# Kernel optimization log

Measured on AMD Instinct MI355X. Metric: run time of the kernel, lower is better.

The kernel has to match this reference:

```python
import jax, jax.numpy as jnp
import numpy as np

D, H = 256, 4            # model dim, num heads
HD = D // H              # head dim (even, needed by rotate_half)
B, N, M, NS = 2, 6, 512, 512  # batch, views, t keypoints, s keypoints
EPS = 1e-5


def _linear(x, w, b):
    return x @ w + b


def _ln(x, g, b):
    mu = x.mean(-1, keepdims=True)
    var = ((x - mu) ** 2).mean(-1, keepdims=True)
    return (x - mu) * jax.lax.rsqrt(var + EPS) * g + b


def _ffn(x, f1w, f1b, lng, lnb, f2w, f2b):
    # Linear(2d,2d) -> LayerNorm -> exact GELU -> Linear(2d,d)
    h = jax.nn.gelu(_ln(_linear(x, f1w, f1b), lng, lnb), approximate=False)
    return _linear(h, f2w, f2b)


def _rotate_half(x):
    # pairs (x0,x1) -> (-x1, x0), interleaved
    return jnp.stack((-x[..., 1::2], x[..., 0::2]), axis=-1).reshape(x.shape)


def _rope(freqs, t):
    return t * freqs[0] + _rotate_half(t) * freqs[1]


def _attn(q, k, v):
    sim = jnp.einsum('...id,...jd->...ij', q, k) * (q.shape[-1] ** -0.5)
    return jnp.einsum('...ij,...jd->...id', jax.nn.softmax(sim, axis=-1), v)


def _self_block(x, enc, qkv_w, qkv_b, out_w, out_b, *ffn_p):
    b, n_img, m, d = x.shape
    enc = jnp.swapaxes(enc, 2, 3)  # encoding.dim()==6 path
    qkv = _linear(x, qkv_w, qkv_b).reshape(b, n_img, m, H, HD, 3)
    qkv = jnp.swapaxes(qkv, -4, -3)  # [b,N,H,m,hd,3]
    q, k, v = qkv[..., 0], qkv[..., 1], qkv[..., 2]
    ctx = _attn(_rope(enc, q), _rope(enc, k), v)  # [b,N,H,m,hd]
    msg = _linear(jnp.swapaxes(ctx, -3, -2).reshape(b, n_img, m, d), out_w, out_b)
    return x + _ffn(jnp.concatenate([x, msg], -1), *ffn_p)


def _t2t_block(t, qkv_w, qkv_b, out_w, out_b, *ffn_p):
    t2 = jnp.swapaxes(t, 1, 2)  # [b,m,N,d]
    b, m, n_img, d = t2.shape
    qkv = _linear(t2, qkv_w, qkv_b).reshape(b, m, n_img, H, HD, 3)
    qkv = jnp.swapaxes(qkv, 3, 2)  # [b,m,H,N,hd,3]
    q, k, v = qkv[..., 0], qkv[..., 1], qkv[..., 2]
    ctx = _attn(q, k, v)  # [b,m,H,N,hd]
    msg = _linear(jnp.swapaxes(ctx, 3, 2).reshape(b, m, n_img, d), out_w, out_b)
    return jnp.swapaxes(t2 + _ffn(jnp.concatenate([t2, msg], -1), *ffn_p), 1, 2)


def _s2s_block(s, q_enc, k_enc, qkv_w, qkv_b, out_w, out_b, *ffn_p):
    b, n_img, n, d = s.shape
    qkv = _linear(s, qkv_w, qkv_b).reshape(b, n_img, n, H, HD, 3)
    qkv = jnp.swapaxes(jnp.swapaxes(qkv, -4, -3), -5, -4)  # [b,H,N,n,hd,3]
    q, k, v = qkv[..., 0], qkv[..., 1], qkv[..., 2]
    # expand queries across all views, RoPE per (i,j) view pair
    q = jnp.broadcast_to(q[:, :, None], (b, H, n_img, n_img, n, HD))
    q = _rope(q_enc, q).reshape(b, H, n_img, n_img * n, HD)
    k = _rope(k_enc, k)
    ctx = _attn(q, k, v).reshape(b, H, n_img, n_img, n, HD)
    # drop diagonal (i==j) entries exactly like boolean-mask indexing in torch
    off = np.nonzero(~np.eye(n_img, dtype=bool).ravel())[0]
    ctx = ctx.reshape(b, H, n_img * n_img, n, HD)[:, :, off]
    ctx = ctx.reshape(b, H, n_img - 1, n_img, n, HD).mean(2)  # [b,H,N,n,hd]
    ctx = jnp.swapaxes(jnp.swapaxes(ctx, 1, 2), 2, 3).reshape(b, n_img, n, d)
    msg = _linear(ctx, out_w, out_b)
    return s + _ffn(jnp.concatenate([s, msg], -1), *ffn_p)


def _cross_block(d0, d1, q_w, q_b, kv_w, kv_b, out_w, out_b, *ffn_p):
    b, n_img, m, d = d0.shape
    m1 = d1.shape[2]
    q = jnp.swapaxes(_linear(d0, q_w, q_b).reshape(b, n_img, m, H, HD), 2, 3)
    kv = jnp.swapaxes(_linear(d1, kv_w, kv_b).reshape(b, n_img, m1, H, HD, 2), 2, 3)
    ctx = _attn(q, kv[..., 0], kv[..., 1])  # [b,N,H,m,hd]
    msg = _linear(jnp.swapaxes(ctx, 2, 3).reshape(b, n_img, m, d), out_w, out_b)
    return d0 + _ffn(jnp.concatenate([d0, msg], -1), *ffn_p)


def setup_inputs() -> dict:
    key = jax.random.key(0)
    ks = iter(jax.random.split(key, 80))
    f32 = jnp.float32

    def lin(din, dout):
        return (jax.random.normal(next(ks), (din, dout), f32) * (din ** -0.5),
                jnp.zeros((dout,), f32))

    inp = {}
    inp['t_desc'] = jax.random.normal(next(ks), (B, N, M, D), f32)
    inp['s_desc'] = jax.random.normal(next(ks), (B, N, NS, D), f32)
    inp['t_encoding'] = jax.random.normal(next(ks), (2, 1, 1, N, M, HD), f32)
    inp['s_encoding'] = jax.random.normal(next(ks), (2, 1, 1, N, NS, HD), f32)
    inp['q_encoding'] = jax.random.normal(next(ks), (2, 1, 1, N, N, 1, HD), f32)
    inp['k_encoding'] = jax.random.normal(next(ks), (2, 1, 1, N, NS, HD), f32)
    for pre in ('sa', 'ss', 'tt'):
        inp[pre + '_qkv_w'], inp[pre + '_qkv_b'] = lin(D, 3 * D)
        inp[pre + '_out_w'], inp[pre + '_out_b'] = lin(D, D)
        inp[pre + '_f1_w'], inp[pre + '_f1_b'] = lin(2 * D, 2 * D)
        inp[pre + '_ln_g'] = jnp.ones((2 * D,), f32)
        inp[pre + '_ln_b'] = jnp.zeros((2 * D,), f32)
        inp[pre + '_f2_w'], inp[pre + '_f2_b'] = lin(2 * D, D)
    inp['ca_q_w'], inp['ca_q_b'] = lin(D, D)
    inp['ca_kv_w'], inp['ca_kv_b'] = lin(D, 2 * D)
    inp['ca_out_w'], inp['ca_out_b'] = lin(D, D)
    inp['ca_f1_w'], inp['ca_f1_b'] = lin(2 * D, 2 * D)
    inp['ca_ln_g'] = jnp.ones((2 * D,), f32)
    inp['ca_ln_b'] = jnp.zeros((2 * D,), f32)
    inp['ca_f2_w'], inp['ca_f2_b'] = lin(2 * D, D)
    inp['cf_w1'], inp['cf_b1'] = lin(D, D)
    inp['cf_w2'], inp['cf_b2'] = lin(D, 1)
    return inp


def reference(t_desc, s_desc, t_encoding, s_encoding, q_encoding, k_encoding,
              sa_qkv_w, sa_qkv_b, sa_out_w, sa_out_b, sa_f1_w, sa_f1_b, sa_ln_g, sa_ln_b, sa_f2_w, sa_f2_b,
              ss_qkv_w, ss_qkv_b, ss_out_w, ss_out_b, ss_f1_w, ss_f1_b, ss_ln_g, ss_ln_b, ss_f2_w, ss_f2_b,
              tt_qkv_w, tt_qkv_b, tt_out_w, tt_out_b, tt_f1_w, tt_f1_b, tt_ln_g, tt_ln_b, tt_f2_w, tt_f2_b,
              ca_q_w, ca_q_b, ca_kv_w, ca_kv_b, ca_out_w, ca_out_b, ca_f1_w, ca_f1_b, ca_ln_g, ca_ln_b, ca_f2_w, ca_f2_b,
              cf_w1, cf_b1, cf_w2, cf_b2):
    sa = (sa_qkv_w, sa_qkv_b, sa_out_w, sa_out_b, sa_f1_w, sa_f1_b, sa_ln_g, sa_ln_b, sa_f2_w, sa_f2_b)
    t = _self_block(t_desc, t_encoding, *sa)   # shared SelfBlock weights
    s = _self_block(s_desc, s_encoding, *sa)
    t = _t2t_block(t, tt_qkv_w, tt_qkv_b, tt_out_w, tt_out_b, tt_f1_w, tt_f1_b, tt_ln_g, tt_ln_b, tt_f2_w, tt_f2_b)
    s = _s2s_block(s, q_encoding, k_encoding, ss_qkv_w, ss_qkv_b, ss_out_w, ss_out_b, ss_f1_w, ss_f1_b, ss_ln_g, ss_ln_b, ss_f2_w, ss_f2_b)
    ca = (ca_q_w, ca_q_b, ca_kv_w, ca_kv_b, ca_out_w, ca_out_b, ca_f1_w, ca_f1_b, ca_ln_g, ca_ln_b, ca_f2_w, ca_f2_b)
    t2 = _cross_block(t, s, *ca)               # shared CrossBlock weights
    s2 = _cross_block(s, t, *ca)
    conf = _linear(jax.nn.relu(_linear(jax.lax.stop_gradient(s), cf_w1, cf_b1)), cf_w2, cf_b2)[..., 0]
    return t2, s2, conf
```

## Files before the change

kernel.cpp:

```cpp
#include <hip/hip_runtime.h>
#include <hip/hip_bf16.h>
#include <math.h>

constexpr int kD   = 256;
constexpr int kH   = 4;
constexpr int kHD  = 64;
constexpr int kB   = 2;
constexpr int kN   = 6;
constexpr int kM   = 512;
constexpr int kRowsH = kB*kN*kM;
constexpr int kRows  = 2*kRowsH;
constexpr int kGrpH  = kB*kN*kH;
constexpr int kGrp   = 2*kGrpH;
constexpr size_t kTOK = (size_t)kRowsH*kD;
constexpr size_t kEncSlab = (size_t)kN*kM*kHD;
constexpr size_t kQEncSlab = (size_t)kN*kN*kHD;
constexpr float kL2E = 1.4426950408889634f;

typedef unsigned short u16;
typedef __attribute__((ext_vector_type(8))) short s16x8;
typedef __attribute__((ext_vector_type(4))) float f32x4;

__device__ __forceinline__ float wred_sum(float v){
  #pragma unroll
  for (int m=32;m>0;m>>=1) v += __shfl_xor(v, m, 64);
  return v;
}
__device__ __forceinline__ u16 f2b(float x){
  union { float f; unsigned u; } a; a.f = x;
  unsigned r = a.u + 0x7fffu + ((a.u >> 16) & 1u);
  return (u16)(r >> 16);
}
__device__ __forceinline__ float b2f(u16 x){
  union { unsigned u; float f; } a; a.u = ((unsigned)x) << 16;
  return a.f;
}
__device__ __forceinline__ unsigned pk2(float lo, float hi){
  union { __hip_bfloat162 h2; unsigned u; } c;
  c.h2 = __float22bfloat162_rn(make_float2(lo, hi));
  return c.u;
}

struct FuseArgs {
  const float* Wout[4]; const float* W1[4];
  const float* bout[4]; const float* b1[4];
  float* Wtmp; float* b1p;
};

__global__ __launch_bounds__(256) void wfuse_k(FuseArgs fa)
{
  if (blockIdx.x >= 128) {
    const int bb = blockIdx.x - 128;
    const int set = bb >> 1;
    const int n = (bb & 1)*256 + threadIdx.x;
    const float* W1 = fa.W1[set];
    const float* bo = fa.bout[set];
    float s = fa.b1[set][n];
    for (int k = 0; k < 256; ++k)
      s = fmaf(bo[k], W1[(size_t)(256+k)*512 + n], s);
    fa.b1p[set*512 + n] = s;
    return;
  }
  const int set = blockIdx.x >> 5;
  const int t = blockIdx.x & 31;
  const int row0 = (t >> 3)*64, col0 = (t & 7)*64;
  const float* A  = fa.Wout[set];
  const float* Bm = fa.W1[set] + 256*512;
  float* C = fa.Wtmp + (size_t)set*(256*512);
  __shared__ float As[16][65];
  __shared__ float Bs[16][64];
  const int tid = threadIdx.x;
  const int tx = tid & 15, ty = tid >> 4;
  const int ar = tid >> 2, ak = (tid & 3)*4;
  const int wr = tid >> 4, wc = (tid & 15)*4;
  float acc[4][4] = {};
  for (int kt = 0; kt < 256; kt += 16) {
    float4 av = *(const float4*)(A + (size_t)(row0+ar)*256 + kt + ak);
    As[ak+0][ar]=av.x; As[ak+1][ar]=av.y; As[ak+2][ar]=av.z; As[ak+3][ar]=av.w;
    *(float4*)(&Bs[wr][wc]) = *(const float4*)(Bm + (size_t)(kt+wr)*512 + col0 + wc);
    __syncthreads();
    #pragma unroll
    for (int k2=0;k2<16;++k2) {
      float a[4], b[4];
      #pragma unroll
      for (int i=0;i<4;++i) a[i]=As[k2][ty*4+i];
      #pragma unroll
      for (int j=0;j<4;++j) b[j]=Bs[k2][tx*4+j];
      #pragma unroll
      for (int i=0;i<4;++i)
        #pragma unroll
        for (int j=0;j<4;++j) acc[i][j] = fmaf(a[i], b[j], acc[i][j]);
    }
    __syncthreads();
  }
  #pragma unroll
  for (int i=0;i<4;++i)
    #pragma unroll
    for (int j=0;j<4;++j)
      C[(size_t)(row0+ty*4+i)*512 + col0+tx*4+j] = acc[i][j];
}

struct WtDesc { const float* W; const float* W2; u16* Wt; int K; int N; int ntiles; };
struct WtTable { WtDesc d[18]; };

__global__ __launch_bounds__(256) void wtcast_k(WtTable tab)
{
  int t = blockIdx.x, mi = 0;
  while (t >= tab.d[mi].ntiles) { t -= tab.d[mi].ntiles; ++mi; }
  const float* W = tab.d[mi].W;
  const float* W2 = tab.d[mi].W2;
  u16* Wt = tab.d[mi].Wt;
  const int K = tab.d[mi].K, N = tab.d[mi].N;
  const int ktn = K >> 5;
  const int nt = t / ktn, kt = t % ktn;
  const int n0 = nt*128, k0 = kt*32;
  u16* dst = Wt + (size_t)t*4096;
  #pragma unroll
  for (int s = 0; s < 2; ++s) {
    const int idx0 = (s*256 + (int)threadIdx.x)*8;
    const int ar = idx0 >> 5;
    const int w8 = (idx0 >> 3) & 3;
    const int sw = (ar >> 1) & 3;
    int kk = k0 + ((w8 ^ sw) << 3);
    const int n  = n0 + ar;
    const float* src = W;
    if (W2 && kk >= 256) { src = W2; kk -= 256; }
    union { u16 u[8]; s16x8 v; } o;
    #pragma unroll
    for (int e = 0; e < 8; ++e)
      o.u[e] = f2b(src[(size_t)(kk + e)*N + n]);
    *(s16x8*)(dst + idx0) = o.v;
  }
}

template<bool A1B, bool A2B, bool CB>
__global__ __launch_bounds__(256) void mmad_k(
    const void* __restrict__ A1a, const void* __restrict__ A1b,
    const void* __restrict__ A2a, const void* __restrict__ A2b, int K1,
    const u16* __restrict__ Wa, const u16* __restrict__ Wb,
    const float* __restrict__ bia, const float* __restrict__ bib,
    const float* __restrict__ bi2a, const float* __restrict__ bi2b, int Ns,
    const float* __restrict__ Ra, const float* __restrict__ Rb,
    void* __restrict__ Cp, int N, int K, int Mh, int doRelu)
{
  __shared__ u16 As[2][128*32];
  __shared__ u16 Bs[2][128*32];
  const int tid = threadIdx.x;
  const int lane = tid & 63, w = tid >> 6;
  const int gx = gridDim.x;
  const int nblk = gx * gridDim.y;
  int flat = blockIdx.y*gx + blockIdx.x;
  if (!(nblk & 7)) flat = (flat & 7)*(nblk >> 3) + (flat >> 3);
  const int bxx = flat % gx, byy = flat / gx;
  const int row0 = byy*128, col0 = bxx*128;
  const bool sec = (row0 >= Mh);
  const int lr0 = sec ? row0 - Mh : row0;
  const void* A1 = sec ? A1b : A1a;
  const void* A2 = sec ? A2b : A2a;
  const u16* Wt  = sec ? Wb : Wa;
  const float* bias  = sec ? bib : bia;
  const float* bias2 = sec ? bi2b : bi2a;
  const float* R = sec ? Rb : Ra;
  const int wr = (w >> 1)*64, wc = (w & 1)*64;
  const int ar = tid >> 1, ah = tid & 1;
  const int K2 = K - K1;
  const int ktn = K >> 5;
  f32x4 acc[4][4] = {};

  auto stage = [&](int buf, int kt) {
    const u16* wtile = Wt + ((size_t)((col0 >> 7)*ktn + (kt >> 5)))*4096;
    #pragma unroll
    for (int s = 0; s < 2; ++s) {
      const u16* srcp = wtile + (size_t)(s*256 + tid)*8;
      __builtin_amdgcn_global_load_lds(
          (const __attribute__((address_space(1))) void*)srcp,
          (__attribute__((address_space(3))) void*)((char*)Bs[buf] + s*4096 + w*1024),
          16, 0, 0);
    }
    const int kk = kt + ah*16;
    union { u16 u[16]; s16x8 v[2]; } tmp;
    if (kk < K1) {
      if constexpr (A1B) {
        const u16* ap = (const u16*)A1 + (size_t)(lr0+ar)*K1 + kk;
        tmp.v[0] = *(const s16x8*)ap; tmp.v[1] = *(const s16x8*)(ap+8);
      } else {
        const float* ap = (const float*)A1 + (size_t)(lr0+ar)*K1 + kk;
        #pragma unroll
        for (int i = 0; i < 16; i += 4) {
          f32x4 v4 = *(const f32x4*)(ap + i);
          tmp.u[i+0]=f2b(v4.x); tmp.u[i+1]=f2b(v4.y); tmp.u[i+2]=f2b(v4.z); tmp.u[i+3]=f2b(v4.w);
        }
      }
    } else {
      if constexpr (A2B) {
        const u16* ap = (const u16*)A2 + (size_t)(lr0+ar)*K2 + (kk - K1);
        tmp.v[0] = *(const s16x8*)ap; tmp.v[1] = *(const s16x8*)(ap+8);
      } else {
        const float* ap = (const float*)A2 + (size_t)(lr0+ar)*K2 + (kk - K1);
        #pragma unroll
        for (int i = 0; i < 16; i += 4) {
          f32x4 v4 = *(const f32x4*)(ap + i);
          tmp.u[i+0]=f2b(v4.x); tmp.u[i+1]=f2b(v4.y); tmp.u[i+2]=f2b(v4.z); tmp.u[i+3]=f2b(v4.w);
        }
      }
    }
    const int sw = (ar >> 1) & 3;
    *(s16x8*)(&As[buf][ar*32 + ((ah*2+0)^sw)*8]) = tmp.v[0];
    *(s16x8*)(&As[buf][ar*32 + ((ah*2+1)^sw)*8]) = tmp.v[1];
  };

  stage(0, 0);
  __syncthreads();
  for (int t = 0; t < ktn; ++t) {
    const int cur = t & 1;
    if (t + 1 < ktn) stage(cur ^ 1, (t + 1) << 5);
    s16x8 af[4], bfv[4];
    #pragma unroll
    for (int fm = 0; fm < 4; ++fm) {
      const int r = wr + fm*16 + (lane & 15);
      const int g = (lane >> 4) ^ ((r >> 1) & 3);
      af[fm] = *(const s16x8*)(&As[cur][r*32 + g*8]);
    }
    #pragma unroll
    for (int fn = 0; fn < 4; ++fn) {
      const int c = wc + fn*16 + (lane & 15);
      const int g = (lane >> 4) ^ ((c >> 1) & 3);
      bfv[fn] = *(const s16x8*)(&Bs[cur][c*32 + g*8]);
    }
    #pragma unroll
    for (int fm = 0; fm < 4; ++fm)
      #pragma unroll
      for (int fn = 0; fn < 4; ++fn)
        acc[fm][fn] = __builtin_amdgcn_mfma_f32_16x16x32_bf16(af[fm], bfv[fn], acc[fm][fn], 0, 0, 0);
    __syncthreads();
  }

  #pragma unroll
  for (int fm = 0; fm < 4; ++fm) {
    const int ro = wr + fm*16 + (lane >> 4)*4;
    #pragma unroll
    for (int fn = 0; fn < 4; ++fn) {
      const int cc = col0 + wc + fn*16 + (lane & 15);
      const float bv = (cc < Ns) ? bias[cc] : bias2[cc - Ns];
      #pragma unroll
      for (int j = 0; j < 4; ++j) {
        float v = acc[fm][fn][j] + bv;
        if (R) v += R[(size_t)(lr0 + ro + j)*N + cc];
        if (doRelu) v = fmaxf(v, 0.f);
        const size_t idx = (size_t)(row0 + ro + j)*N + cc;
        if constexpr (CB) ((u16*)Cp)[idx] = f2b(v);
        else              ((float*)Cp)[idx] = v;
      }
    }
  }
}

__global__ __launch_bounds__(256) void prep_self_k(
    const u16* __restrict__ qkvU, const float* __restrict__ t_enc,
    const float* __restrict__ s_enc,
    u16* __restrict__ Qb, u16* __restrict__ Kb, u16* __restrict__ Vt)
{
  __shared__ u16 vs[64][66];
  const int g = blockIdx.x >> 3, i0 = (blockIdx.x & 7)*64;
  const int h = g & 3, bn = g >> 2;
  const float* enc = (bn < 12) ? t_enc : s_enc;
  const int n = (bn < 12 ? bn : bn - 12) % kN;
  const int c = threadIdx.x & 63, t4 = threadIdx.x >> 6;
  const float sgn = (c & 1) ? 1.f : -1.f;
  #pragma unroll 4
  for (int rr = 0; rr < 16; ++rr) {
    const int il = rr*4 + t4, i = i0 + il;
    const u16* base = qkvU + ((size_t)bn*kM + i)*768 + h*192;
    const float q = b2f(base[c*3]), k = b2f(base[c*3+1]);
    const float qp = b2f(base[(c^1)*3]), kp = b2f(base[(c^1)*3+1]);
    const size_t eo = ((size_t)(n*kM + i))*kHD + c;
    const float e0 = enc[eo], e1 = enc[kEncSlab + eo];
    Qb[((size_t)g*kM + i)*kHD + c] = f2b((q*e0 + sgn*qp*e1)*0.125f);
    Kb[((size_t)g*kM + i)*kHD + c] = f2b(k*e0 + sgn*kp*e1);
    vs[il][c] = base[c*3+2];
  }
  __syncthreads();
  #pragma unroll 4
  for (int rr = 0; rr < 16; ++rr) {
    const int cc = rr*4 + t4;
    Vt[((size_t)g*kHD + cc)*kM + i0 + c] = vs[c][cc];
  }
}

__global__ __launch_bounds__(256) void prep_s2s_k(
    const u16* __restrict__ qkvU, const float* __restrict__ kenc,
    float* __restrict__ Qs, u16* __restrict__ Kb, u16* __restrict__ Vt)
{
  __shared__ u16 vs[64][66];
  const int g = blockIdx.x >> 3, i0 = (blockIdx.x & 7)*64;
  const int view = g % kN, bh = g / kN;
  const int h = bh & 3, b = bh >> 2;
  const int c = threadIdx.x & 63, t4 = threadIdx.x >> 6;
  const float sgn = (c & 1) ? 1.f : -1.f;
  #pragma unroll 4
  for (int rr = 0; rr < 16; ++rr) {
    const int il = rr*4 + t4, i = i0 + il;
    const u16* base = qkvU + ((size_t)(kRowsH + (b*kN+view)*kM + i))*768 + h*192;
    const float k = b2f(base[c*3+1]), kp = b2f(base[(c^1)*3+1]);
    const size_t eo = ((size_t)(view*kM + i))*kHD + c;
    const float e0 = kenc[eo], e1 = kenc[kEncSlab + eo];
    Qs[((size_t)g*kM + i)*kHD + c] = b2f(base[c*3]);
    Kb[((size_t)g*kM + i)*kHD + c] = f2b(k*e0 + sgn*kp*e1);
    vs[il][c] = base[c*3+2];
  }
  __syncthreads();
  #pragma unroll 4
  for (int rr = 0; rr < 16; ++rr) {
    const int cc = rr*4 + t4;
    Vt[((size_t)g*kHD + cc)*kM + i0 + c] = vs[c][cc];
  }
}

__global__ __launch_bounds__(256) void prep_cross_k(
    const u16* __restrict__ qkvC, u16* __restrict__ Kb, u16* __restrict__ Vt)
{
  __shared__ u16 vs[64][66];
  const int g = blockIdx.x >> 3, i0 = (blockIdx.x & 7)*64;
  const int h = g & 3, bn = g >> 2;
  const int src = (bn < 12) ? bn + 12 : bn - 12;
  const int c = threadIdx.x & 63, t4 = threadIdx.x >> 6;
  #pragma unroll 4
  for (int rr = 0; rr < 16; ++rr) {
    const int il = rr*4 + t4, i = i0 + il;
    const u16* base = qkvC + ((size_t)src*kM + i)*768 + 256 + h*128;
    Kb[((size_t)g*kM + i)*kHD + c] = f2b(b2f(base[c*2]) * 0.125f);
    vs[il][c] = base[c*2+1];
  }
  __syncthreads();
  #pragma unroll 4
  for (int rr = 0; rr < 16; ++rr) {
    const int cc = rr*4 + t4;
    Vt[((size_t)g*kHD + cc)*kM + i0 + c] = vs[c][cc];
  }
}

template<int CROSSQ>
__global__ __launch_bounds__(256) void attn_mm_k(
    const u16* __restrict__ Qb, const u16* __restrict__ Kb,
    const u16* __restrict__ Vt, u16* __restrict__ ctx)
{
  const int w = threadIdx.x >> 6, lane = threadIdx.x & 63;
  const int bij = (blockIdx.x & 7)*48 + (blockIdx.x >> 3);
  const int g = bij >> 2, qblk = bij & 3;
  const int h = g & 3, bn = g >> 2;
  const int q0 = qblk*128 + w*32;
  const int qr = lane & 15, hi = lane >> 4;
  const bool subhi = (hi & 1), up = (hi >= 2);

  s16x8 qf0[2], qf1[2];
  #pragma unroll
  for (int f = 0; f < 2; ++f) {
    const u16* qp = CROSSQ
      ? Qb + ((size_t)(bn*kM + q0 + f*16 + qr))*768 + h*kHD + hi*8
      : Qb + ((size_t)g*kM + q0 + f*16 + qr)*kHD + hi*8;
    qf0[f] = *(const s16x8*)(qp);
    qf1[f] = *(const s16x8*)(qp + 32);
  }

  const u16* Kg = Kb + (size_t)g*kM*kHD;
  const u16* Vg = Vt + (size_t)g*kHD*kM;
  f32x4 acc[2][4] = {};
  float m[2] = {-1e30f, -1e30f}, l[2] = {0.f, 0.f};

  s16x8 kA[2][2], kB[2][2];
  f32x4 sA[2][2], sB[2][2];

  auto loadK = [&](s16x8 kb[2][2], int kc){
    #pragma unroll
    for (int t = 0; t < 2; ++t) {
      const u16* kp = Kg + ((size_t)(kc*32 + t*16 + qr))*kHD + hi*8;
      kb[t][0] = *(const s16x8*)(kp);
      kb[t][1] = *(const s16x8*)(kp + 32);
    }
  };
  auto qk = [&](const s16x8 kb[2][2], f32x4 st[2][2]){
    #pragma unroll
    for (int f = 0; f < 2; ++f)
      #pragma unroll
      for (int t = 0; t < 2; ++t) {
        f32x4 z = {0.f, 0.f, 0.f, 0.f};
        z = __builtin_amdgcn_mfma_f32_16x16x32_bf16(kb[t][0], qf0[f], z, 0, 0, 0);
        z = __builtin_amdgcn_mfma_f32_16x16x32_bf16(kb[t][1], qf1[f], z, 0, 0, 0);
        st[f][t] = z;
      }
  };
  auto smpv = [&](f32x4 st[2][2], int kc){
    const int k0 = kc*32;
    s16x8 pa[2];
    #pragma unroll
    for (int f = 0; f < 2; ++f) {
      float mloc = fmaxf(fmaxf(fmaxf(st[f][0][0], st[f][0][1]), fmaxf(st[f][0][2], st[f][0][3])),
                         fmaxf(fmaxf(st[f][1][0], st[f][1][1]), fmaxf(st[f][1][2], st[f][1][3])));
      if (!__all(mloc - m[f] <= 8.f)) {
        mloc = fmaxf(mloc, __shfl_xor(mloc, 16));
        mloc = fmaxf(mloc, __shfl_xor(mloc, 32));
        const float mn = fmaxf(m[f], mloc);
        const float r = exp2f((m[f] - mn)*kL2E);
        m[f] = mn;
        l[f] *= r;
        const float rr0 = __shfl(r, hi*4+0), rr1 = __shfl(r, hi*4+1);
        const float rr2 = __shfl(r, hi*4+2), rr3 = __shfl(r, hi*4+3);
        #pragma unroll
        for (int db = 0; db < 4; ++db) {
          acc[f][db][0] *= rr0; acc[f][db][1] *= rr1;
          acc[f][db][2] *= rr2; acc[f][db][3] *= rr3;
        }
      }
      float p[8], ls = 0.f;
      #pragma unroll
      for (int t = 0; t < 2; ++t)
        #pragma unroll
        for (int j = 0; j < 4; ++j) {
          const float pv = exp2f((st[f][t][j] - m[f])*kL2E);
          p[t*4+j] = pv; ls += pv;
        }
      l[f] += ls;
      const unsigned c00 = pk2(p[0], p[1]);
      const unsigned c01 = pk2(p[2], p[3]);
      const unsigned c10 = pk2(p[4], p[5]);
      const unsigned c11 = pk2(p[6], p[7]);
      const unsigned c00x = __shfl_xor((int)c00, 32), c10x = __shfl_xor((int)c10, 32);
      const unsigned c01x = __shfl_xor((int)c01, 32), c11x = __shfl_xor((int)c11, 32);
      const unsigned E = up ? c10x : c00, F = up ? c10 : c00x;
      const unsigned G = up ? c11x : c01, H = up ? c11 : c01x;
      const unsigned Ex = __shfl_xor((int)E, 16), Fx = __shfl_xor((int)F, 16);
      const unsigned Gx = __shfl_xor((int)G, 16), Hx = __shfl_xor((int)H, 16);
      union { unsigned w[4]; s16x8 v; } pw;
      pw.w[0] = subhi ? Fx : E;
      pw.w[1] = subhi ? Hx : G;
      pw.w[2] = subhi ? F  : Ex;
      pw.w[3] = subhi ? H  : Gx;
      pa[f] = pw.v;
    }
    #pragma unroll
    for (int db = 0; db < 4; ++db) {
      const s16x8 vf = *(const s16x8*)(Vg + ((size_t)(db*16 + qr))*kM + k0 + hi*8);
      acc[0][db] = __builtin_amdgcn_mfma_f32_16x16x32_bf16(pa[0], vf, acc[0][db], 0, 0, 0);
      acc[1][db] = __builtin_amdgcn_mfma_f32_16x16x32_bf16(pa[1], vf, acc[1][db], 0, 0, 0);
    }
  };

  loadK(kA, 0);
  qk(kA, sA);
  loadK(kB, 1);
  for (int kc = 0; kc < 16; kc += 2) {
    qk(kB, sB);
    if (kc + 2 < 16) loadK(kA, kc + 2);
    smpv(sA, kc);
    if (kc + 2 < 16) qk(kA, sA);
    if (kc + 3 < 16) loadK(kB, kc + 3);
    smpv(sB, kc + 1);
  }

  #pragma unroll
  for (int f = 0; f < 2; ++f) {
    float lf = l[f];
    lf += __shfl_xor(lf, 16); lf += __shfl_xor(lf, 32);
    const float li = 1.f/lf;
    const float l0 = __shfl(li, hi*4+0), l1 = __shfl(li, hi*4+1);
    const float l2 = __shfl(li, hi*4+2), l3 = __shfl(li, hi*4+3);
    #pragma unroll
    for (int db = 0; db < 4; ++db) {
      const size_t base = ((size_t)(bn*kM + q0 + f*16 + hi*4))*kD + h*kHD + db*16 + qr;
      ctx[base + 0*kD] = f2b(acc[f][db][0]*l0);
      ctx[base + 1*kD] = f2b(acc[f][db][1]*l1);
      ctx[base + 2*kD] = f2b(acc[f][db][2]*l2);
      ctx[base + 3*kD] = f2b(acc[f][db][3]*l3);
    }
  }
}

__device__ __forceinline__ void rope4(const f32x4 x, const f32x4 e0, const f32x4 e1, float o[4])
{
  o[0] = x[0]*e0[0] - x[1]*e1[0];
  o[1] = x[1]*e0[1] + x[0]*e1[1];
  o[2] = x[2]*e0[2] - x[3]*e1[2];
  o[3] = x[3]*e0[3] + x[2]*e1[3];
}

__global__ __launch_bounds__(256) void attn_comb_k(
    const float* __restrict__ Qraw, const u16* __restrict__ Kb,
    const u16* __restrict__ Vt, const float* __restrict__ qenc,
    u16* __restrict__ ctx5, const u16* __restrict__ qkvU,
    u16* __restrict__ ctxU)
{
  if (blockIdx.x >= 960) {
    const int wid = (blockIdx.x - 960)*4 + ((int)threadIdx.x >> 6);
    const int lane = threadIdx.x & 63;
    const int mm2 = wid & 511;
    const int t = wid >> 9;
    const int nq = t % kN;
    const int bh2 = t / kN;
    const int h2 = bh2 & 3, b2 = bh2 >> 2;
    const u16* pb[kN];
    #pragma unroll
    for (int nk = 0; nk < kN; ++nk)
      pb[nk] = qkvU + ((size_t)(b2*kN+nk)*kM + mm2)*768 + h2*192;
    const float qc = b2f(pb[nq][lane*3]);
    float sim[kN];
    #pragma unroll
    for (int nk = 0; nk < kN; ++nk)
      sim[nk] = wred_sum(qc * b2f(pb[nk][lane*3+1])) * 0.125f;
    float mx = sim[0];
    #pragma unroll
    for (int nk = 1; nk < kN; ++nk) mx = fmaxf(mx, sim[nk]);
    float p[kN], s = 0.f;
    #pragma unroll
    for (int nk = 0; nk < kN; ++nk) { p[nk] = expf(sim[nk]-mx); s += p[nk]; }
    const float inv = 1.f/s;
    float o = 0.f;
    #pragma unroll
    for (int nk = 0; nk < kN; ++nk) o = fmaf(p[nk], b2f(pb[nk][lane*3+2]), o);
    ctxU[((size_t)(b2*kN+nq)*kM + mm2)*kD + h2*kHD + lane] = f2b(o*inv);
    return;
  }
  const int w = threadIdx.x >> 6, lane = threadIdx.x & 63;
  const int bij = (blockIdx.x & 7)*120 + (blockIdx.x >> 3);
  const int bh = bij / 120;
  const int rest = bij % 120;
  const int col = rest / 20;
  const int rem = rest % 20;
  const int qblk = rem / 5, split = rem % 5;
  const int q0 = qblk*128 + w*32;
  const int qr = lane & 15, hi = lane >> 4;
  const bool subhi = (hi & 1), up = (hi >= 2);

  const int e  = split*6 + col;
  const int iv = e/5;
  const int j0 = e%5;
  const int jv = j0 + (j0 >= iv ? 1 : 0);

  s16x8 qf0[2], qf1[2];
  #pragma unroll
  for (int f = 0; f < 2; ++f) {
    const float* qp = Qraw + ((size_t)(bh*kN + jv)*kM + q0 + f*16 + qr)*kHD + hi*8;
    const float* ep = qenc + ((size_t)(iv*kN + jv))*kHD + hi*8;
    union { u16 u[8]; s16x8 v; } A, B;
    float o[4];
    rope4(*(const f32x4*)(qp),   *(const f32x4*)(ep),   *(const f32x4*)(ep+kQEncSlab), o);
    #pragma unroll
    for (int j = 0; j < 4; ++j) A.u[j] = f2b(o[j]*0.125f);
    rope4(*(const f32x4*)(qp+4), *(const f32x4*)(ep+4), *(const f32x4*)(ep+kQEncSlab+4), o);
    #pragma unroll
    for (int j = 0; j < 4; ++j) A.u[4+j] = f2b(o[j]*0.125f);
    rope4(*(const f32x4*)(qp+32), *(const f32x4*)(ep+32), *(const f32x4*)(ep+kQEncSlab+32), o);
    #pragma unroll
    for (int j = 0; j < 4; ++j) B.u[j] = f2b(o[j]*0.125f);
    rope4(*(const f32x4*)(qp+36), *(const f32x4*)(ep+36), *(const f32x4*)(ep+kQEncSlab+36), o);
    #pragma unroll
    for (int j = 0; j < 4; ++j) B.u[4+j] = f2b(o[j]*0.125f);
    qf0[f] = A.v; qf1[f] = B.v;
  }

  const int g2 = bh*kN + iv;
  const u16* Kg = Kb + (size_t)g2*kM*kHD;
  const u16* Vg = Vt + (size_t)g2*kHD*kM;
  f32x4 acc[2][4] = {};
  float m[2] = {-1e30f, -1e30f}, l[2] = {0.f, 0.f};

  s16x8 kA[2][2], kB2[2][2];
  f32x4 sA[2][2], sB[2][2];

  auto loadK = [&](s16x8 kb[2][2], int kc){
    #pragma unroll
    for (int t = 0; t < 2; ++t) {
      const u16* kp = Kg + ((size_t)(kc*32 + t*16 + qr))*kHD + hi*8;
      kb[t][0] = *(const s16x8*)(kp);
      kb[t][1] = *(const s16x8*)(kp + 32);
    }
  };
  auto qk = [&](const s16x8 kb[2][2], f32x4 st[2][2]){
    #pragma unroll
    for (int f = 0; f < 2; ++f)
      #pragma unroll
      for (int t = 0; t < 2; ++t) {
        f32x4 z = {0.f, 0.f, 0.f, 0.f};
        z = __builtin_amdgcn_mfma_f32_16x16x32_bf16(kb[t][0], qf0[f], z, 0, 0, 0);
        z = __builtin_amdgcn_mfma_f32_16x16x32_bf16(kb[t][1], qf1[f], z, 0, 0, 0);
        st[f][t] = z;
      }
  };
  auto smpv = [&](f32x4 st[2][2], int kc){
    const int k0 = kc*32;
    s16x8 pa[2];
    #pragma unroll
    for (int f = 0; f < 2; ++f) {
      float mloc = fmaxf(fmaxf(fmaxf(st[f][0][0], st[f][0][1]), fmaxf(st[f][0][2], st[f][0][3])),
                         fmaxf(fmaxf(st[f][1][0], st[f][1][1]), fmaxf(st[f][1][2], st[f][1][3])));
      if (!__all(mloc - m[f] <= 8.f)) {
        mloc = fmaxf(mloc, __shfl_xor(mloc, 16));
        mloc = fmaxf(mloc, __shfl_xor(mloc, 32));
        const float mn = fmaxf(m[f], mloc);
        const float r = exp2f((m[f] - mn)*kL2E);
        m[f] = mn;
        l[f] *= r;
        const float rr0 = __shfl(r, hi*4+0), rr1 = __shfl(r, hi*4+1);
        const float rr2 = __shfl(r, hi*4+2), rr3 = __shfl(r, hi*4+3);
        #pragma unroll
        for (int db = 0; db < 4; ++db) {
          acc[f][db][0] *= rr0; acc[f][db][1] *= rr1;
          acc[f][db][2] *= rr2; acc[f][db][3] *= rr3;
        }
      }
      float p[8], ls = 0.f;
      #pragma unroll
      for (int t = 0; t < 2; ++t)
        #pragma unroll
        for (int j = 0; j < 4; ++j) {
          const float pv = exp2f((st[f][t][j] - m[f])*kL2E);
          p[t*4+j] = pv; ls += pv;
        }
      l[f] += ls;
      const unsigned c00 = pk2(p[0], p[1]);
      const unsigned c01 = pk2(p[2], p[3]);
      const unsigned c10 = pk2(p[4], p[5]);
      const unsigned c11 = pk2(p[6], p[7]);
      const unsigned c00x = __shfl_xor((int)c00, 32), c10x = __shfl_xor((int)c10, 32);
      const unsigned c01x = __shfl_xor((int)c01, 32), c11x = __shfl_xor((int)c11, 32);
      const unsigned E = up ? c10x : c00, F = up ? c10 : c00x;
      const unsigned G = up ? c11x : c01, H = up ? c11 : c01x;
      const unsigned Ex = __shfl_xor((int)E, 16), Fx = __shfl_xor((int)F, 16);
      const unsigned Gx = __shfl_xor((int)G, 16), Hx = __shfl_xor((int)H, 16);
      union { unsigned w[4]; s16x8 v; } pw;
      pw.w[0] = subhi ? Fx : E;
      pw.w[1] = subhi ? Hx : G;
      pw.w[2] = subhi ? F  : Ex;
      pw.w[3] = subhi ? H  : Gx;
      pa[f] = pw.v;
    }
    #pragma unroll
    for (int db = 0; db < 4; ++db) {
      const s16x8 vf = *(const s16x8*)(Vg + ((size_t)(db*16 + qr))*kM + k0 + hi*8);
      acc[0][db] = __builtin_amdgcn_mfma_f32_16x16x32_bf16(pa[0], vf, acc[0][db], 0, 0, 0);
      acc[1][db] = __builtin_amdgcn_mfma_f32_16x16x32_bf16(pa[1], vf, acc[1][db], 0, 0, 0);
    }
  };

  loadK(kA, 0);
  qk(kA, sA);
  loadK(kB2, 1);
  for (int kc = 0; kc < 16; kc += 2) {
    qk(kB2, sB);
    if (kc + 2 < 16) loadK(kA, kc + 2);
    smpv(sA, kc);
    if (kc + 2 < 16) qk(kA, sA);
    if (kc + 3 < 16) loadK(kB2, kc + 3);
    smpv(sB, kc + 1);
  }

  const int b = bh >> 2, h = bh & 3;
  u16* outp = ctx5 + (size_t)split*kTOK;
  #pragma unroll
  for (int f = 0; f < 2; ++f) {
    float lf = l[f];
    lf += __shfl_xor(lf, 16); lf += __shfl_xor(lf, 32);
    const float li = 0.2f/lf;
    const float l0 = __shfl(li, hi*4+0), l1 = __shfl(li, hi*4+1);
    const float l2 = __shfl(li, hi*4+2), l3 = __shfl(li, hi*4+3);
    #pragma unroll
    for (int db = 0; db < 4; ++db) {
      const size_t base = ((size_t)((b*kN + col)*kM + q0 + f*16 + hi*4))*kD + h*kHD + db*16 + qr;
      outp[base + 0*kD] = f2b(acc[f][db][0]*l0);
      outp[base + 1*kD] = f2b(acc[f][db][1]*l1);
      outp[base + 2*kD] = f2b(acc[f][db][2]*l2);
      outp[base + 3*kD] = f2b(acc[f][db][3]*l3);
    }
  }
}

__global__ __launch_bounds__(256) void sum5_k(const u16* __restrict__ c5,
                                              u16* __restrict__ outU)
{
  const size_t i4 = ((size_t)blockIdx.x*256 + threadIdx.x)*4;
  float s0=0.f, s1=0.f, s2=0.f, s3=0.f;
  #pragma unroll
  for (int sp = 0; sp < 5; ++sp) {
    uint2 d = *(const uint2*)(c5 + sp*kTOK + i4);
    s0 += b2f((u16)(d.x & 0xffff)); s1 += b2f((u16)(d.x >> 16));
    s2 += b2f((u16)(d.y & 0xffff)); s3 += b2f((u16)(d.y >> 16));
  }
  union { u16 u[4]; uint2 d; } o;
  o.u[0]=f2b(s0); o.u[1]=f2b(s1); o.u[2]=f2b(s2); o.u[3]=f2b(s3);
  *(uint2*)(outU + i4) = o.d;
}

__global__ __launch_bounds__(256) void lngelu_k(
    const u16* __restrict__ x, u16* __restrict__ y,
    const float* __restrict__ g0, const float* __restrict__ b0,
    const float* __restrict__ g1, const float* __restrict__ b1, int Mh)
{
  const int w = threadIdx.x >> 6, lane = threadIdx.x & 63;
  const int row = blockIdx.x*4 + w;
  const float* g = (row < Mh) ? g0 : g1;
  const float* bb = (row < Mh) ? b0 : b1;
  const int o8 = lane*8;
  union { u16 u[8]; s16x8 v; } xv;
  xv.v = *(const s16x8*)(x + (size_t)row*512 + o8);
  float vf[8];
  float s1 = 0.f, s2 = 0.f;
  #pragma unroll
  for (int j = 0; j < 8; ++j) {
    vf[j] = b2f(xv.u[j]);
    s1 += vf[j]; s2 += vf[j]*vf[j];
  }
  s1 = wred_sum(s1); s2 = wred_sum(s2);
  const float mean = s1 * (1.f/512.f);
  const float ms   = s2 * (1.f/512.f);
  const float rs = rsqrtf(ms - mean*mean + 1e-5f);
  f32x4 gv0 = *(const f32x4*)(g + o8),  gv1 = *(const f32x4*)(g + o8 + 4);
  f32x4 bv0 = *(const f32x4*)(bb + o8), bv1 = *(const f32x4*)(bb + o8 + 4);
  union { u16 u[8]; s16x8 v; } ov;
  #pragma unroll
  for (int j = 0; j < 8; ++j) {
    const float gj = (j < 4) ? gv0[j] : gv1[j-4];
    const float bj = (j < 4) ? bv0[j] : bv1[j-4];
    const float yv = (vf[j]-mean)*rs*gj + bj;
    ov.u[j] = f2b(0.5f*yv*(1.f+erff(yv*0.70710678118654752f)));
  }
  *(s16x8*)(y + (size_t)row*512 + o8) = ov.v;
}

__global__ void conf_dot_k(const float* __restrict__ tmp, const float* __restrict__ w2,
                           const float* __restrict__ b2, float* __restrict__ out)
{
  const int w = threadIdx.x >> 6, lane = threadIdx.x & 63;
  const int row = blockIdx.x*4 + w;
  const float* t = tmp + (size_t)row*kD;
  float s = 0.f;
  #pragma unroll
  for (int j=0;j<4;++j) s = fmaf(t[lane+j*64], w2[lane+j*64], s);
  s = wred_sum(s);
  if (lane == 0) out[row] = s + b2[0];
}

extern "C" void kernel_launch(void* const* d_in, const int* in_sizes, int n_in,
                              void* d_out, int out_size, void* d_ws, size_t ws_size,
                              hipStream_t stream)
{
  auto F = [&](int i){ return (const float*)d_in[i]; };
  const float* t_desc = F(0);
  const float* s_desc = F(1);
  const float* t_enc  = F(2);
  const float* s_enc  = F(3);
  const float* q_enc  = F(4);
  const float* k_enc  = F(5);

  char* base = (char*)d_ws;
  float* xts = (float*)base;
  float* xt = xts;
  float* xs = xts + kTOK;
  char* R1  = base + 2*kTOK*sizeof(float);
  char* CTX = R1 + 4*kTOK*sizeof(float);
  char* MSG = CTX + 2*kTOK*sizeof(u16);
  u16* Qb16 = (u16*)(MSG + kTOK*sizeof(float));
  u16* Kb16 = Qb16 + 2*kTOK;
  u16* Vt16 = Kb16 + 2*kTOK;
  u16* wsW  = Vt16 + 2*kTOK;
  u16*   qkvU  = (u16*)R1;
  u16*   yH    = (u16*)R1;
  u16*   ctx5  = qkvU + (size_t)kRowsH*768;
  float* Wtmp  = (float*)R1;
  u16*   ctxU  = (u16*)CTX;
  float* Qs2s  = (float*)MSG;
  float* confb = (float*)MSG;
  u16*   yU    = (u16*)CTX;

  float* out_t2s2 = (float*)d_out;
  float* out_conf = (float*)d_out + 2*kTOK;

  WtTable tab;
  int nd = 0, total_tiles = 0;
  size_t woff = 0;
  const u16* wp[18];
  auto addw = [&](int idx, const float* W2, int K, int N){
    u16* dst = wsW + woff;
    tab.d[nd] = { F(idx), W2, dst, K, N, (N>>7)*(K>>5) };
    total_tiles += tab.d[nd].ntiles;
    wp[nd] = dst;
    woff += (size_t)K*N;
    ++nd;
    return nd-1;
  };
  const int W_SA_QKV = addw(6,  nullptr, 256, 768);
  const int W_SA_F1  = addw(10, Wtmp + 0*131072, 512, 512);
  const int W_SA_F2  = addw(14, nullptr, 512, 256);
  const int W_SS_QKV = addw(16, nullptr, 256, 768);
  const int W_SS_F1  = addw(20, Wtmp + 1*131072, 512, 512);
  const int W_SS_F2  = addw(24, nullptr, 512, 256);
  const int W_TT_QKV = addw(26, nullptr, 256, 768);
  const int W_TT_F1  = addw(30, Wtmp + 2*131072, 512, 512);
  const int W_TT_F2  = addw(34, nullptr, 512, 256);
  const int W_CA_Q   = addw(36, nullptr, 256, 256);
  const int W_CA_KV  = addw(38, nullptr, 256, 512);
  const int W_CA_F1  = addw(42, Wtmp + 3*131072, 512, 512);
  const int W_CA_F2  = addw(46, nullptr, 512, 256);
  const int W_CF_1   = addw(48, nullptr, 256, 256);
  (void)W_CA_KV;
  float* b1p = (float*)(wsW + woff);

  FuseArgs fa;
  fa.Wout[0]=F(8);  fa.Wout[1]=F(18); fa.Wout[2]=F(28); fa.Wout[3]=F(40);
  fa.W1[0]=F(10);   fa.W1[1]=F(20);   fa.W1[2]=F(30);   fa.W1[3]=F(42);
  fa.bout[0]=F(9);  fa.bout[1]=F(19); fa.bout[2]=F(29); fa.bout[3]=F(41);
  fa.b1[0]=F(11);   fa.b1[1]=F(21);   fa.b1[2]=F(31);   fa.b1[3]=F(43);
  fa.Wtmp = Wtmp; fa.b1p = b1p;
  wfuse_k<<<136, 256, 0, stream>>>(fa);
  wtcast_k<<<total_tiles, 256, 0, stream>>>(tab);

  auto mm_f32_to_b16 = [&](const float* a1a, const float* a1b, int wa, int wb2,
                           const float* ba, const float* bb2, u16* c, int N_, int K_){
    dim3 grid(N_/128, kRows/128);
    mmad_k<false,false,true><<<grid,256,0,stream>>>(a1a, a1b, nullptr, nullptr, K_,
        wp[wa], wp[wb2], ba, bb2, ba, bb2, N_, nullptr, nullptr, c, N_, K_, kRowsH, 0);
  };
  auto mm_f1 = [&](const float* a1a, const float* a1b, const u16* a2a, const u16* a2b,
                   int wa, int wb2, const float* ba, const float* bb2, u16* c){
    dim3 grid(512/128, kRows/128);
    mmad_k<false,true,true><<<grid,256,0,stream>>>(a1a, a1b, a2a, a2b, 256,
        wp[wa], wp[wb2], ba, bb2, ba, bb2, 512, nullptr, nullptr, c, 512, 512, kRowsH, 0);
  };
  auto mm_f2 = [&](const u16* a1a, const u16* a1b, int wa, int wb2,
                   const float* ba, const float* bb2,
                   const float* ra, const float* rb, float* c){
    dim3 grid(256/128, kRows/128);
    mmad_k<true,false,false><<<grid,256,0,stream>>>(a1a, a1b, nullptr, nullptr, 512,
        wp[wa], wp[wb2], ba, bb2, ba, bb2, 256, ra, rb, c, 256, 512, kRowsH, 0);
  };

  mm_f32_to_b16(t_desc, s_desc, W_SA_QKV, W_SA_QKV, F(7), F(7), qkvU, 768, 256);
  prep_self_k<<<kGrp*8, 256, 0, stream>>>(qkvU, t_enc, s_enc, Qb16, Kb16, Vt16);
  attn_mm_k<0><<<384, 256, 0, stream>>>(Qb16, Kb16, Vt16, ctxU);
  mm_f1(t_desc, s_desc, ctxU, ctxU + kTOK, W_SA_F1, W_SA_F1, b1p+0*512, b1p+0*512, yH);
  lngelu_k<<<kRows/4, 256, 0, stream>>>(yH, yU, F(12), F(13), F(12), F(13), kRowsH);
  mm_f2(yU, yU + (size_t)kRowsH*512, W_SA_F2, W_SA_F2, F(15), F(15), t_desc, s_desc, xts);

  mm_f32_to_b16(xt, xs, W_TT_QKV, W_SS_QKV, F(27), F(17), qkvU, 768, 256);
  prep_s2s_k<<<kGrpH*8, 256, 0, stream>>>(qkvU, k_enc, Qs2s, Kb16, Vt16);
  attn_comb_k<<<960 + 6144, 256, 0, stream>>>(Qs2s, Kb16, Vt16, q_enc, ctx5, qkvU, ctxU);
  sum5_k<<<(int)(kTOK/1024), 256, 0, stream>>>(ctx5, ctxU + kTOK);
  mm_f1(xt, xs, ctxU, ctxU + kTOK, W_TT_F1, W_SS_F1, b1p+2*512, b1p+1*512, yH);
  lngelu_k<<<kRows/4, 256, 0, stream>>>(yH, yU, F(32), F(33), F(22), F(23), kRowsH);
  mm_f2(yU, yU + (size_t)kRowsH*512, W_TT_F2, W_SS_F2, F(35), F(25), xt, xs, xts);

  {
    dim3 grid(2, kRowsH/128);
    mmad_k<false,false,false><<<grid,256,0,stream>>>(xs, xs, nullptr, nullptr, 256,
        wp[W_CF_1], wp[W_CF_1], F(49), F(49), F(49), F(49), 256,
        nullptr, nullptr, confb, 256, 256, kRowsH, 1);
  }
  conf_dot_k<<<kRowsH/4, 256, 0, stream>>>(confb, F(50), F(51), out_conf);

  {
    dim3 grid(768/128, kRows/128);
    mmad_k<false,false,true><<<grid,256,0,stream>>>(xt, xs, nullptr, nullptr, 256,
        wp[W_CA_Q], wp[W_CA_Q], F(37), F(37), F(39), F(39), 256,
        nullptr, nullptr, qkvU, 768, 256, kRowsH, 0);
  }
  prep_cross_k<<<kGrp*8, 256, 0, stream>>>(qkvU, Kb16, Vt16);
  attn_mm_k<1><<<384, 256, 0, stream>>>(qkvU, Kb16, Vt16, ctxU);
  mm_f1(xt, xs, ctxU, ctxU + kTOK, W_CA_F1, W_CA_F1, b1p+3*512, b1p+3*512, yH);
  lngelu_k<<<kRows/4, 256, 0, stream>>>(yH, yU, F(44), F(45), F(44), F(45), kRowsH);
  mm_f2(yU, yU + (size_t)kRowsH*512, W_CA_F2, W_CA_F2, F(47), F(47), xt, xs, out_t2s2);
}
```

Baseline: 460.2 us.

## Double query rows per wave in s2s attention and drop K software pipelining

Each wave in the s2s attention part of attn_comb_k now handles 64 query rows (four 16-row fragments) instead of 32, which halves the attention block count and reuses each loaded K/V fragment across twice as many MFMAs. The hand-written two-stage K prefetch pipeline is replaced by a simple per-chunk loop. This cuts K/V global reads per query but raises register pressure, lowers parallelism (480 attention blocks), and loses the explicit load/compute overlap.

```diff
diff --git a/kernel.cpp b/kernel.cpp
--- a/kernel.cpp
+++ b/kernel.cpp
@@ -489,8 +489,8 @@
     u16* __restrict__ ctx5, const u16* __restrict__ qkvU,
     u16* __restrict__ ctxU)
 {
-  if (blockIdx.x >= 960) {
-    const int wid = (blockIdx.x - 960)*4 + ((int)threadIdx.x >> 6);
+  if (blockIdx.x >= 480) {
+    const int wid = (blockIdx.x - 480)*4 + ((int)threadIdx.x >> 6);
     const int lane = threadIdx.x & 63;
     const int mm2 = wid & 511;
     const int t = wid >> 9;
@@ -520,13 +520,13 @@
     return;
   }
   const int w = threadIdx.x >> 6, lane = threadIdx.x & 63;
-  const int bij = (blockIdx.x & 7)*120 + (blockIdx.x >> 3);
-  const int bh = bij / 120;
-  const int rest = bij % 120;
-  const int col = rest / 20;
-  const int rem = rest % 20;
+  const int bij = (blockIdx.x & 7)*60 + (blockIdx.x >> 3);
+  const int bh = bij / 60;
+  const int rest = bij % 60;
+  const int col = rest / 10;
+  const int rem = rest % 10;
   const int qblk = rem / 5, split = rem % 5;
-  const int q0 = qblk*128 + w*32;
+  const int q0 = qblk*256 + w*64;
   const int qr = lane & 15, hi = lane >> 4;
   const bool subhi = (hi & 1), up = (hi >= 2);
 
@@ -535,9 +535,9 @@
   const int j0 = e%5;
   const int jv = j0 + (j0 >= iv ? 1 : 0);
 
-  s16x8 qf0[2], qf1[2];
-  #pragma unroll
-  for (int f = 0; f < 2; ++f) {
+  s16x8 qf0[4], qf1[4];
+  #pragma unroll
+  for (int f = 0; f < 4; ++f) {
     const float* qp = Qraw + ((size_t)(bh*kN + jv)*kM + q0 + f*16 + qr)*kHD + hi*8;
     const float* ep = qenc + ((size_t)(iv*kN + jv))*kHD + hi*8;
     union { u16 u[8]; s16x8 v; } A, B;
@@ -560,38 +560,31 @@
   const int g2 = bh*kN + iv;
   const u16* Kg = Kb + (size_t)g2*kM*kHD;
   const u16* Vg = Vt + (size_t)g2*kHD*kM;
-  f32x4 acc[2][4] = {};
-  float m[2] = {-1e30f, -1e30f}, l[2] = {0.f, 0.f};
-
-  s16x8 kA[2][2], kB2[2][2];
-  f32x4 sA[2][2], sB[2][2];
-
-  auto loadK = [&](s16x8 kb[2][2], int kc){
+  f32x4 acc[4][4] = {};
+  float m[4] = {-1e30f, -1e30f, -1e30f, -1e30f}, l[4] = {0.f, 0.f, 0.f, 0.f};
+
+  for (int kc = 0; kc < 16; ++kc) {
+    const int k0 = kc*32;
+    s16x8 a0[2], a1[2];
     #pragma unroll
     for (int t = 0; t < 2; ++t) {
-      const u16* kp = Kg + ((size_t)(kc*32 + t*16 + qr))*kHD + hi*8;
-      kb[t][0] = *(const s16x8*)(kp);
-      kb[t][1] = *(const s16x8*)(kp + 32);
-    }
-  };
-  auto qk = [&](const s16x8 kb[2][2], f32x4 st[2][2]){
-    #pragma unroll
-    for (int f = 0; f < 2; ++f)
+      const u16* kp = Kg + ((size_t)(k0 + t*16 + qr))*kHD + hi*8;
+      a0[t] = *(const s16x8*)(kp);
+      a1[t] = *(const s16x8*)(kp + 32);
+    }
+    s16x8 pa[4];
+    #pragma unroll
+    for (int f = 0; f < 4; ++f) {
+      f32x4 st[2];
       #pragma unroll
       for (int t = 0; t < 2; ++t) {
         f32x4 z = {0.f, 0.f, 0.f, 0.f};
-        z = __builtin_amdgcn_mfma_f32_16x16x32_bf16(kb[t][0], qf0[f], z, 0, 0, 0);
-        z = __builtin_amdgcn_mfma_f32_16x16x32_bf16(kb[t][1], qf1[f], z, 0, 0, 0);
-        st[f][t] = z;
+        z = __builtin_amdgcn_mfma_f32_16x16x32_bf16(a0[t], qf0[f], z, 0, 0, 0);
+        z = __builtin_amdgcn_mfma_f32_16x16x32_bf16(a1[t], qf1[f], z, 0, 0, 0);
+        st[t] = z;
       }
-  };
-  auto smpv = [&](f32x4 st[2][2], int kc){
-    const int k0 = kc*32;
-    s16x8 pa[2];
-    #pragma unroll
-    for (int f = 0; f < 2; ++f) {
-      float mloc = fmaxf(fmaxf(fmaxf(st[f][0][0], st[f][0][1]), fmaxf(st[f][0][2], st[f][0][3])),
-                         fmaxf(fmaxf(st[f][1][0], st[f][1][1]), fmaxf(st[f][1][2], st[f][1][3])));
+      float mloc = fmaxf(fmaxf(fmaxf(st[0][0], st[0][1]), fmaxf(st[0][2], st[0][3])),
+                         fmaxf(fmaxf(st[1][0], st[1][1]), fmaxf(st[1][2], st[1][3])));
       if (!__all(mloc - m[f] <= 8.f)) {
         mloc = fmaxf(mloc, __shfl_xor(mloc, 16));
         mloc = fmaxf(mloc, __shfl_xor(mloc, 32));
@@ -612,7 +605,7 @@
       for (int t = 0; t < 2; ++t)
         #pragma unroll
         for (int j = 0; j < 4; ++j) {
-          const float pv = exp2f((st[f][t][j] - m[f])*kL2E);
+          const float pv = exp2f((st[t][j] - m[f])*kL2E);
           p[t*4+j] = pv; ls += pv;
         }
       l[f] += ls;
@@ -636,27 +629,16 @@
     #pragma unroll
     for (int db = 0; db < 4; ++db) {
       const s16x8 vf = *(const s16x8*)(Vg + ((size_t)(db*16 + qr))*kM + k0 + hi*8);
-      acc[0][db] = __builtin_amdgcn_mfma_f32_16x16x32_bf16(pa[0], vf, acc[0][db], 0, 0, 0);
-      acc[1][db] = __builtin_amdgcn_mfma_f32_16x16x32_bf16(pa[1], vf, acc[1][db], 0, 0, 0);
-    }
-  };
-
-  loadK(kA, 0);
-  qk(kA, sA);
-  loadK(kB2, 1);
-  for (int kc = 0; kc < 16; kc += 2) {
-    qk(kB2, sB);
-    if (kc + 2 < 16) loadK(kA, kc + 2);
-    smpv(sA, kc);
-    if (kc + 2 < 16) qk(kA, sA);
-    if (kc + 3 < 16) loadK(kB2, kc + 3);
-    smpv(sB, kc + 1);
+      #pragma unroll
+      for (int f = 0; f < 4; ++f)
+        acc[f][db] = __builtin_amdgcn_mfma_f32_16x16x32_bf16(pa[f], vf, acc[f][db], 0, 0, 0);
+    }
   }
 
   const int b = bh >> 2, h = bh & 3;
   u16* outp = ctx5 + (size_t)split*kTOK;
   #pragma unroll
-  for (int f = 0; f < 2; ++f) {
+  for (int f = 0; f < 4; ++f) {
     float lf = l[f];
     lf += __shfl_xor(lf, 16); lf += __shfl_xor(lf, 32);
     const float li = 0.2f/lf;
@@ -841,7 +823,7 @@
 
   mm_f32_to_b16(xt, xs, W_TT_QKV, W_SS_QKV, F(27), F(17), qkvU, 768, 256);
   prep_s2s_k<<<kGrpH*8, 256, 0, stream>>>(qkvU, k_enc, Qs2s, Kb16, Vt16);
-  attn_comb_k<<<960 + 6144, 256, 0, stream>>>(Qs2s, Kb16, Vt16, q_enc, ctx5, qkvU, ctxU);
+  attn_comb_k<<<480 + 6144, 256, 0, stream>>>(Qs2s, Kb16, Vt16, q_enc, ctx5, qkvU, ctxU);
   sum5_k<<<(int)(kTOK/1024), 256, 0, stream>>>(ctx5, ctxU + kTOK);
   mm_f1(xt, xs, ctxU, ctxU + kTOK, W_TT_F1, W_SS_F1, b1p+2*512, b1p+1*512, yH);
   lngelu_k<<<kRows/4, 256, 0, stream>>>(yH, yU, F(32), F(33), F(22), F(23), kRowsH);
```

Measured after the change: 442.9 us (median of 2 runs). 1.04x faster.
